# Kernel optimization log

Hardware: AMD Instinct MI355X
Metric: run time of the kernel (lower is better)

The kernel has to match this reference:

```python
import jax, jax.numpy as jnp
import numpy as np

DN = ('NCHW', 'OIHW', 'NCHW')

def _convlstm_scan(x, W, b):
    """x: [S,B,Cin,H,W]; W: [4*Co, Cin+Co, 3, 3]; b: [4*Co]. Returns all h: [S,B,Co,H,W]."""
    S, B, Cin, H, Wd = x.shape
    Co = W.shape[0] // 4
    h0 = jnp.zeros((B, Co, H, Wd), x.dtype)
    c0 = jnp.zeros((B, Co, H, Wd), x.dtype)

    def step(carry, xt):
        h, c = carry
        z = jax.lax.conv_general_dilated(
            jnp.concatenate([xt, h], axis=1), W,
            window_strides=(1, 1), padding='SAME', dimension_numbers=DN)
        z = z + b[None, :, None, None]
        i, f, o, g = jnp.split(z, 4, axis=1)
        c = jax.nn.sigmoid(f) * c + jax.nn.sigmoid(i) * jnp.tanh(g)
        h = jax.nn.sigmoid(o) * jnp.tanh(c)
        return (h, c), h

    _, outs = jax.lax.scan(step, (h0, c0), x)
    return outs


def setup_inputs() -> dict:
    key = jax.random.key(0)
    k1, k2, k3 = jax.random.split(key, 3)
    S, B, C, H, W = 16, 4, 32, 128, 128
    Co = 32
    x = jax.random.normal(k1, (S, B, C, H, W), dtype=jnp.float32)
    Wf = jax.random.normal(k2, (4 * Co, C + Co, 3, 3), dtype=jnp.float32) * 0.05
    bf = jnp.zeros((4 * Co,), dtype=jnp.float32)
    Wb = jax.random.normal(k3, (4 * Co, C + Co, 3, 3), dtype=jnp.float32) * 0.05
    bb = jnp.zeros((4 * Co,), dtype=jnp.float32)
    return {"x": x, "Wf": Wf, "bf": bf, "Wb": Wb, "bb": bb}


def reference(x, Wf, bf, Wb, bb):
    fwd_outs = _convlstm_scan(x, Wf, bf)            # [S,B,Co,H,W]
    bwd_outs = _convlstm_scan(x[::-1], Wb, bb)      # [S,B,Co,H,W] (time-reversed input)
    # Faithful to source: backward outputs concatenated WITHOUT re-flipping.
    return jnp.concatenate([fwd_outs, bwd_outs], axis=2)  # [S,B,2*Co,H,W]
```

## Files before the change

### kernel.cpp

```cpp
#include <hip/hip_runtime.h>

#define S_ 16
#define B_ 4
#define H_ 128
#define W_ 128
#define HW_ (H_ * W_)
#define NPOS 324
#define TILE_ELEMS (NPOS * 32)

typedef __attribute__((ext_vector_type(8))) _Float16 half8;
typedef __attribute__((ext_vector_type(4))) _Float16 half4;
typedef __attribute__((ext_vector_type(4))) float f32x4;

__device__ __forceinline__ float sigf(float x) { return 1.f / (1.f + __expf(-x)); }
__device__ __forceinline__ float tanhf_(float x) { return 2.f / (1.f + __expf(-2.f * x)) - 1.f; }

__device__ __forceinline__ void gl2lds16(const _Float16* g, _Float16* l) {
    __builtin_amdgcn_global_load_lds(
        (const __attribute__((address_space(1))) unsigned int*)g,
        (__attribute__((address_space(3))) unsigned int*)l, 16, 0, 0);
}

__global__ void prep_pack(const float* __restrict__ Wf, const float* __restrict__ Wb,
                          _Float16* __restrict__ wpk) {
    int id = blockIdx.x * 256 + threadIdx.x;
    if (id >= 18432) return;
    int l = id & 63;
    int nf = (id >> 6) & 7;
    int ks = (id >> 9) % 18;
    int d = id / 9216;
    const float* Wsrc = d ? Wb : Wf;
    int tap = ks >> 1, half = ks & 1;
    int dy = tap / 3, dx = tap - dy * 3;
    int co = nf * 16 + (l & 15);
    _Float16* dst = wpk + (size_t)d * 73728 + ((size_t)(ks * 8 + nf) * 64 + l) * 8;
#pragma unroll
    for (int e = 0; e < 8; ++e) {
        int ci = half * 32 + (l >> 4) * 8 + e;
        dst[e] = (_Float16)Wsrc[((co * 64 + ci) * 3 + dy) * 3 + dx];
    }
}

__global__ void prep_xtiles(const float* __restrict__ x, _Float16* __restrict__ xt) {
    int id = blockIdx.x * 256 + threadIdx.x;
    if (id >= 16 * 4 * 64 * NPOS * 4) return;
    int cb = id & 3;
    int u = id >> 2;
    int pos = u % NPOS;
    int v = u / NPOS;
    int tile = v & 63;
    v >>= 6;
    int b = v & 3;
    int ts = v >> 2;
    int r = pos / 18, cc = pos - r * 18;
    int gy = (tile >> 3) * 16 + r - 1;
    int gx = (tile & 7) * 16 + cc - 1;
    bool inb = ((unsigned)gy < 128u) && ((unsigned)gx < 128u);
    const float* g = x + ((size_t)(ts * 4 + b) * 32 + cb * 8) * HW_ + (size_t)gy * W_ + gx;
    half8 vv;
#pragma unroll
    for (int e = 0; e < 8; ++e)
        vv[e] = inb ? (_Float16)__builtin_nontemporal_load(g + e * HW_) : (_Float16)0.f;
    *(half8*)(xt + (size_t)u * 32 + cb * 8) = vv;
}

__device__ __forceinline__ half8 lda(const _Float16* __restrict__ base, int m, int dy,
                                     int dx, int px, int kg, int wq) {
    return *(const half8*)(base + (size_t)(((wq * 4 + m + dy) * 18) + px + dx) * 32 + kg * 8);
}
__device__ __forceinline__ half8 ldb(const _Float16* __restrict__ bw, int ks, int nf, int lane) {
    return *(const half8*)(bw + (size_t)(ks * 8 + nf) * 512 + lane * 8);
}

__global__ __launch_bounds__(256, 2)
void convlstm_step(const _Float16* __restrict__ xtiles,
                   const _Float16* __restrict__ hin,
                   _Float16* __restrict__ hout,
                   const _Float16* __restrict__ wpk,
                   const float* __restrict__ biasf, const float* __restrict__ biasb,
                   _Float16* __restrict__ cst,
                   float* __restrict__ out, int t) {
    const int tile = blockIdx.x;
    const int dirb = blockIdx.y;
    const int dir = dirb >> 2, b = dirb & 3;
    const int ts = dir ? (S_ - 1 - t) : t;

    const _Float16* base_x = xtiles + ((size_t)(ts * 4 + b) * 64 + tile) * TILE_ELEMS;
    const _Float16* base_h = hin + ((size_t)dirb * 64 + tile) * TILE_ELEMS;
    _Float16* hob = hout + (size_t)dirb * 64 * TILE_ELEMS;
    const _Float16* bw = wpk + (size_t)dir * 73728;
    const float* bias = dir ? biasb : biasf;
    _Float16* cbase = cst + (size_t)dirb * 32 * HW_;
    float* outp = out + ((size_t)(t * 4 + b) * 64 + dir * 32) * HW_;

    __shared__ alignas(16) _Float16 bsh[2][2][8][64][8];

    const int tid = threadIdx.x;
    const int lane = tid & 63, wq = tid >> 6;
    const int px = lane & 15, kg = lane >> 4;

    f32x4 acc[4][8];
#pragma unroll
    for (int m = 0; m < 4; ++m)
#pragma unroll
        for (int nf = 0; nf < 8; ++nf) acc[m][nf] = (f32x4)(0.f);

    if (t == 0) {
#pragma unroll 1
        for (int tap = 0; tap < 9; ++tap) {
            int dy = tap / 3, dx = tap - dy * 3;
            half8 a[4];
#pragma unroll
            for (int m = 0; m < 4; ++m) a[m] = lda(base_x, m, dy, dx, px, kg, wq);
#pragma unroll
            for (int nf = 0; nf < 8; ++nf) {
                half8 bb8 = ldb(bw, tap * 2, nf, lane);
#pragma unroll
                for (int m = 0; m < 4; ++m)
                    acc[m][nf] = __builtin_amdgcn_mfma_f32_16x16x32_f16(a[m], bb8, acc[m][nf], 0, 0, 0);
            }
        }
    } else {
        half8 aP[2][4], aQ[2][4];
        {
#pragma unroll
            for (int j = 0; j < 4; ++j) {
                int f = wq * 4 + j;
                int hf = f >> 3, nf = f & 7;
                gl2lds16(bw + (size_t)(hf * 8 + nf) * 512 + lane * 8, &bsh[0][hf][nf][0][0]);
            }
#pragma unroll
            for (int m = 0; m < 4; ++m) {
                aP[0][m] = lda(base_x, m, 0, 0, px, kg, wq);
                aP[1][m] = lda(base_h, m, 0, 0, px, kg, wq);
            }
        }

        auto body = [&](int tap, half8(&acur)[2][4], half8(&anxt)[2][4]) {
            __syncthreads();
            if (tap < 8) {
                const int tn = tap + 1;
                const int dyn_ = tn / 3, dxn = tn - dyn_ * 3;
#pragma unroll
                for (int j = 0; j < 4; ++j) {
                    int f = wq * 4 + j;
                    int hf = f >> 3, nf = f & 7;
                    gl2lds16(bw + (size_t)((tn * 2 + hf) * 8 + nf) * 512 + lane * 8,
                             &bsh[tn & 1][hf][nf][0][0]);
                }
#pragma unroll
                for (int m = 0; m < 4; ++m) {
                    anxt[0][m] = lda(base_x, m, dyn_, dxn, px, kg, wq);
                    anxt[1][m] = lda(base_h, m, dyn_, dxn, px, kg, wq);
                }
            }
            const _Float16* lb = &bsh[tap & 1][0][0][0][0];
#pragma unroll
            for (int hf = 0; hf < 2; ++hf) {
#pragma unroll
                for (int nf = 0; nf < 8; ++nf) {
                    half8 bb8 = *(const half8*)(lb + (size_t)(hf * 8 + nf) * 512 + lane * 8);
#pragma unroll
                    for (int m = 0; m < 4; ++m)
                        acc[m][nf] = __builtin_amdgcn_mfma_f32_16x16x32_f16(acur[hf][m], bb8, acc[m][nf], 0, 0, 0);
                }
            }
        };
#pragma unroll 1
        for (int tap = 0; tap < 9; tap += 2) {
            body(tap, aP, aQ);
            if (tap + 1 < 9) body(tap + 1, aQ, aP);
        }
    }

    const int q0 = px;
    const int gx0 = (tile & 7) * 16, gy0 = (tile >> 3) * 16;
    const int tx = tile & 7, ty_ = tile >> 3;
    const int lx0 = kg * 4;

    float bI[2], bF[2], bO[2], bG[2];
#pragma unroll
    for (int qs = 0; qs < 2; ++qs) {
        bI[qs] = bias[qs * 16 + q0];
        bF[qs] = bias[32 + qs * 16 + q0];
        bO[qs] = bias[64 + qs * 16 + q0];
        bG[qs] = bias[96 + qs * 16 + q0];
    }
#pragma unroll
    for (int m = 0; m < 4; ++m) {
        const int ly = wq * 4 + m;
        const int gy = gy0 + ly;
#pragma unroll
        for (int qs = 0; qs < 2; ++qs) {
            const int q = qs * 16 + q0;
            f32x4 zi = acc[m][qs], zf = acc[m][2 + qs], zo = acc[m][4 + qs], zg = acc[m][6 + qs];
            size_t off = (size_t)q * HW_ + (size_t)gy * W_ + gx0 + lx0;
            half4 cold4 = (half4)((_Float16)0.f);
            if (t) cold4 = *(const half4*)(cbase + off);
            half4 cn4;
            f32x4 hn;
#pragma unroll
            for (int r = 0; r < 4; ++r) {
                float I = sigf(zi[r] + bI[qs]);
                float F = sigf(zf[r] + bF[qs]);
                float O = sigf(zo[r] + bO[qs]);
                float G = tanhf_(zg[r] + bG[qs]);
                float cnr = F * (float)cold4[r] + I * G;
                cn4[r] = (_Float16)cnr;
                hn[r] = O * tanhf_(cnr);
            }
            *(half4*)(cbase + off) = cn4;
            __builtin_nontemporal_store(hn, (f32x4*)(outp + off));
#pragma unroll
            for (int r = 0; r < 4; ++r) {
                _Float16 hh = (_Float16)hn[r];
                int lx = lx0 + r;
                hob[((size_t)tile) * TILE_ELEMS + (size_t)((ly + 1) * 18 + lx + 1) * 32 + q] = hh;
                bool Le = (lx == 0) && (tx > 0);
                bool Re = (lx == 15) && (tx < 7);
                bool Te = (ly == 0) && (ty_ > 0);
                bool Be = (ly == 15) && (ty_ < 7);
                if (Le) hob[((size_t)tile - 1) * TILE_ELEMS + (size_t)((ly + 1) * 18 + 17) * 32 + q] = hh;
                if (Re) hob[((size_t)tile + 1) * TILE_ELEMS + (size_t)((ly + 1) * 18 + 0) * 32 + q] = hh;
                if (Te) hob[((size_t)tile - 8) * TILE_ELEMS + (size_t)(17 * 18 + lx + 1) * 32 + q] = hh;
                if (Be) hob[((size_t)tile + 8) * TILE_ELEMS + (size_t)(0 * 18 + lx + 1) * 32 + q] = hh;
                if (Te && Le) hob[((size_t)tile - 9) * TILE_ELEMS + (size_t)(17 * 18 + 17) * 32 + q] = hh;
                if (Te && Re) hob[((size_t)tile - 7) * TILE_ELEMS + (size_t)(17 * 18 + 0) * 32 + q] = hh;
                if (Be && Le) hob[((size_t)tile + 7) * TILE_ELEMS + (size_t)(0 * 18 + 17) * 32 + q] = hh;
                if (Be && Re) hob[((size_t)tile + 9) * TILE_ELEMS + (size_t)(0 * 18 + 0) * 32 + q] = hh;
            }
        }
    }
}

extern "C" void kernel_launch(void* const* d_in, const int* in_sizes, int n_in,
                              void* d_out, int out_size, void* d_ws, size_t ws_size,
                              hipStream_t stream) {
    const float* x  = (const float*)d_in[0];
    const float* Wf = (const float*)d_in[1];
    const float* bf = (const float*)d_in[2];
    const float* Wb = (const float*)d_in[3];
    const float* bb = (const float*)d_in[4];
    float* out = (float*)d_out;
    char* ws = (char*)d_ws;

    const size_t OFF_WPK = 0;
    const size_t OFF_XT  = 327680;
    const size_t OFF_H0  = OFF_XT + 84934656;
    const size_t OFF_H1  = OFF_H0 + 10616832;
    const size_t OFF_C   = OFF_H1 + 10616832;

    _Float16* wpk = (_Float16*)(ws + OFF_WPK);
    _Float16* xt  = (_Float16*)(ws + OFF_XT);
    _Float16* hb[2] = { (_Float16*)(ws + OFF_H0), (_Float16*)(ws + OFF_H1) };
    _Float16* cst = (_Float16*)(ws + OFF_C);

    hipMemsetAsync(ws + OFF_H0, 0, 2u * 10616832u, stream);

    prep_pack<<<dim3(72), dim3(256), 0, stream>>>(Wf, Wb, wpk);
    prep_xtiles<<<dim3(20736), dim3(256), 0, stream>>>(x, xt);

    for (int t = 0; t < S_; ++t) {
        convlstm_step<<<dim3(64, 8), dim3(256), 0, stream>>>(
            xt, hb[(t + 1) & 1], hb[t & 1], wpk, bf, bb, cst, out, t);
    }
}
```

Before: 683.6 us.

## Widen tiles to 16x32 with 512 threads and preload full weights into LDS

Spatial tiles grow from 16x16 to 16x32 pixels, so the halo overhead in the padded x and h tiles shrinks and there are half as many blocks, each with 8 waves. All 18 weight k-slices (144KB) are copied into dynamic LDS once at kernel start, which removes the per-tap barriers and the double-buffered weight streaming. The A operands are prefetched four slices ahead in registers. In exchange only one block fits per CU, and the grid is 256 blocks, so occupancy and latency hiding go down while register pressure goes up.

```diff
diff --git a/kernel.cpp b/kernel.cpp
--- a/kernel.cpp
+++ b/kernel.cpp
@@ -5,7 +5,9 @@
 #define H_ 128
 #define W_ 128
 #define HW_ (H_ * W_)
-#define NPOS 324
+#define AH 18
+#define AW 34
+#define NPOS (AH * AW)
 #define TILE_ELEMS (NPOS * 32)
 
 typedef __attribute__((ext_vector_type(8))) _Float16 half8;
@@ -43,18 +45,18 @@
 
 __global__ void prep_xtiles(const float* __restrict__ x, _Float16* __restrict__ xt) {
     int id = blockIdx.x * 256 + threadIdx.x;
-    if (id >= 16 * 4 * 64 * NPOS * 4) return;
+    if (id >= 16 * 4 * 32 * NPOS * 4) return;
     int cb = id & 3;
     int u = id >> 2;
     int pos = u % NPOS;
     int v = u / NPOS;
-    int tile = v & 63;
-    v >>= 6;
+    int tile = v & 31;
+    v >>= 5;
     int b = v & 3;
     int ts = v >> 2;
-    int r = pos / 18, cc = pos - r * 18;
-    int gy = (tile >> 3) * 16 + r - 1;
-    int gx = (tile & 7) * 16 + cc - 1;
+    int ar = pos / AW, ac = pos - ar * AW;
+    int gy = (tile >> 2) * 16 + ar - 1;
+    int gx = (tile & 3) * 32 + ac - 1;
     bool inb = ((unsigned)gy < 128u) && ((unsigned)gx < 128u);
     const float* g = x + ((size_t)(ts * 4 + b) * 32 + cb * 8) * HW_ + (size_t)gy * W_ + gx;
     half8 vv;
@@ -64,15 +66,15 @@
     *(half8*)(xt + (size_t)u * 32 + cb * 8) = vv;
 }
 
-__device__ __forceinline__ half8 lda(const _Float16* __restrict__ base, int m, int dy,
+__device__ __forceinline__ half8 lda(const _Float16* __restrict__ base, int f, int dy,
                                      int dx, int px, int kg, int wq) {
-    return *(const half8*)(base + (size_t)(((wq * 4 + m + dy) * 18) + px + dx) * 32 + kg * 8);
-}
-__device__ __forceinline__ half8 ldb(const _Float16* __restrict__ bw, int ks, int nf, int lane) {
-    return *(const half8*)(bw + (size_t)(ks * 8 + nf) * 512 + lane * 8);
-}
-
-__global__ __launch_bounds__(256, 2)
+    int pos = (wq * 2 + (f >> 1) + dy) * AW + (f & 1) * 16 + px + dx;
+    return *(const half8*)(base + (size_t)pos * 32 + kg * 8);
+}
+
+extern __shared__ _Float16 bsh[];
+
+__global__ __launch_bounds__(512, 1)
 void convlstm_step(const _Float16* __restrict__ xtiles,
                    const _Float16* __restrict__ hin,
                    _Float16* __restrict__ hout,
@@ -85,97 +87,91 @@
     const int dir = dirb >> 2, b = dirb & 3;
     const int ts = dir ? (S_ - 1 - t) : t;
 
-    const _Float16* base_x = xtiles + ((size_t)(ts * 4 + b) * 64 + tile) * TILE_ELEMS;
-    const _Float16* base_h = hin + ((size_t)dirb * 64 + tile) * TILE_ELEMS;
-    _Float16* hob = hout + (size_t)dirb * 64 * TILE_ELEMS;
+    const _Float16* base_x = xtiles + ((size_t)(ts * 4 + b) * 32 + tile) * TILE_ELEMS;
+    const _Float16* base_h = hin + ((size_t)dirb * 32 + tile) * TILE_ELEMS;
+    _Float16* hob = hout + (size_t)dirb * 32 * TILE_ELEMS;
     const _Float16* bw = wpk + (size_t)dir * 73728;
     const float* bias = dir ? biasb : biasf;
     _Float16* cbase = cst + (size_t)dirb * 32 * HW_;
     float* outp = out + ((size_t)(t * 4 + b) * 64 + dir * 32) * HW_;
 
-    __shared__ alignas(16) _Float16 bsh[2][2][8][64][8];
-
     const int tid = threadIdx.x;
     const int lane = tid & 63, wq = tid >> 6;
     const int px = lane & 15, kg = lane >> 4;
 
+#pragma unroll
+    for (int k = 0; k < 18; ++k) {
+        int wb = k * 512 + (tid & ~63);
+        gl2lds16(bw + ((size_t)wb + lane) * 8, bsh + (size_t)wb * 8);
+    }
+
     f32x4 acc[4][8];
 #pragma unroll
-    for (int m = 0; m < 4; ++m)
-#pragma unroll
-        for (int nf = 0; nf < 8; ++nf) acc[m][nf] = (f32x4)(0.f);
+    for (int f = 0; f < 4; ++f)
+#pragma unroll
+        for (int nf = 0; nf < 8; ++nf) acc[f][nf] = (f32x4)(0.f);
+
+    half8 abuf[4][4];
 
     if (t == 0) {
-#pragma unroll 1
+#pragma unroll
+        for (int tp = 0; tp < 4; ++tp) {
+            int dy = tp / 3, dx = tp - dy * 3;
+#pragma unroll
+            for (int f = 0; f < 4; ++f) abuf[tp][f] = lda(base_x, f, dy, dx, px, kg, wq);
+        }
+        __syncthreads();
+#pragma unroll
         for (int tap = 0; tap < 9; ++tap) {
-            int dy = tap / 3, dx = tap - dy * 3;
-            half8 a[4];
-#pragma unroll
-            for (int m = 0; m < 4; ++m) a[m] = lda(base_x, m, dy, dx, px, kg, wq);
+            const int slot = tap & 3;
 #pragma unroll
             for (int nf = 0; nf < 8; ++nf) {
-                half8 bb8 = ldb(bw, tap * 2, nf, lane);
-#pragma unroll
-                for (int m = 0; m < 4; ++m)
-                    acc[m][nf] = __builtin_amdgcn_mfma_f32_16x16x32_f16(a[m], bb8, acc[m][nf], 0, 0, 0);
+                half8 b8 = *(const half8*)(bsh + ((size_t)((tap * 2) * 8 + nf) << 9) + (lane << 3));
+#pragma unroll
+                for (int f = 0; f < 4; ++f)
+                    acc[f][nf] = __builtin_amdgcn_mfma_f32_16x16x32_f16(abuf[slot][f], b8, acc[f][nf], 0, 0, 0);
+            }
+            if (tap + 4 < 9) {
+                const int tn = tap + 4;
+                const int dyn_ = tn / 3, dxn = tn - dyn_ * 3;
+#pragma unroll
+                for (int f = 0; f < 4; ++f) abuf[slot][f] = lda(base_x, f, dyn_, dxn, px, kg, wq);
             }
         }
     } else {
-        half8 aP[2][4], aQ[2][4];
-        {
-#pragma unroll
-            for (int j = 0; j < 4; ++j) {
-                int f = wq * 4 + j;
-                int hf = f >> 3, nf = f & 7;
-                gl2lds16(bw + (size_t)(hf * 8 + nf) * 512 + lane * 8, &bsh[0][hf][nf][0][0]);
-            }
-#pragma unroll
-            for (int m = 0; m < 4; ++m) {
-                aP[0][m] = lda(base_x, m, 0, 0, px, kg, wq);
-                aP[1][m] = lda(base_h, m, 0, 0, px, kg, wq);
-            }
-        }
-
-        auto body = [&](int tap, half8(&acur)[2][4], half8(&anxt)[2][4]) {
-            __syncthreads();
-            if (tap < 8) {
-                const int tn = tap + 1;
+#pragma unroll
+        for (int k0 = 0; k0 < 4; ++k0) {
+            int tp = k0 >> 1;
+            int dy = tp / 3, dx = tp - dy * 3;
+            const _Float16* src = (k0 & 1) ? base_h : base_x;
+#pragma unroll
+            for (int f = 0; f < 4; ++f) abuf[k0][f] = lda(src, f, dy, dx, px, kg, wq);
+        }
+        __syncthreads();
+#pragma unroll
+        for (int ks = 0; ks < 18; ++ks) {
+            const int slot = ks & 3;
+#pragma unroll
+            for (int nf = 0; nf < 8; ++nf) {
+                half8 b8 = *(const half8*)(bsh + ((size_t)(ks * 8 + nf) << 9) + (lane << 3));
+#pragma unroll
+                for (int f = 0; f < 4; ++f)
+                    acc[f][nf] = __builtin_amdgcn_mfma_f32_16x16x32_f16(abuf[slot][f], b8, acc[f][nf], 0, 0, 0);
+            }
+            if (ks + 4 < 18) {
+                const int kn = ks + 4;
+                const int tn = kn >> 1;
                 const int dyn_ = tn / 3, dxn = tn - dyn_ * 3;
-#pragma unroll
-                for (int j = 0; j < 4; ++j) {
-                    int f = wq * 4 + j;
-                    int hf = f >> 3, nf = f & 7;
-                    gl2lds16(bw + (size_t)((tn * 2 + hf) * 8 + nf) * 512 + lane * 8,
-                             &bsh[tn & 1][hf][nf][0][0]);
-                }
-#pragma unroll
-                for (int m = 0; m < 4; ++m) {
-                    anxt[0][m] = lda(base_x, m, dyn_, dxn, px, kg, wq);
-                    anxt[1][m] = lda(base_h, m, dyn_, dxn, px, kg, wq);
-                }
-            }
-            const _Float16* lb = &bsh[tap & 1][0][0][0][0];
-#pragma unroll
-            for (int hf = 0; hf < 2; ++hf) {
-#pragma unroll
-                for (int nf = 0; nf < 8; ++nf) {
-                    half8 bb8 = *(const half8*)(lb + (size_t)(hf * 8 + nf) * 512 + lane * 8);
-#pragma unroll
-                    for (int m = 0; m < 4; ++m)
-                        acc[m][nf] = __builtin_amdgcn_mfma_f32_16x16x32_f16(acur[hf][m], bb8, acc[m][nf], 0, 0, 0);
-                }
-            }
-        };
-#pragma unroll 1
-        for (int tap = 0; tap < 9; tap += 2) {
-            body(tap, aP, aQ);
-            if (tap + 1 < 9) body(tap + 1, aQ, aP);
+                const _Float16* src = (kn & 1) ? base_h : base_x;
+#pragma unroll
+                for (int f = 0; f < 4; ++f) abuf[slot][f] = lda(src, f, dyn_, dxn, px, kg, wq);
+            }
         }
     }
 
     const int q0 = px;
-    const int gx0 = (tile & 7) * 16, gy0 = (tile >> 3) * 16;
-    const int tx = tile & 7, ty_ = tile >> 3;
+    const int gx0 = (tile & 3) * 32, gy0 = (tile >> 2) * 16;
+    const int tx = tile & 3, ty_ = tile >> 2;
     const int lx0 = kg * 4;
 
     float bI[2], bF[2], bO[2], bG[2];
@@ -187,14 +183,15 @@
         bG[qs] = bias[96 + qs * 16 + q0];
     }
 #pragma unroll
-    for (int m = 0; m < 4; ++m) {
-        const int ly = wq * 4 + m;
-        const int gy = gy0 + ly;
+    for (int f = 0; f < 4; ++f) {
+        const int row = wq * 2 + (f >> 1);
+        const int gy = gy0 + row;
+        const int colb = (f & 1) * 16 + lx0;
 #pragma unroll
         for (int qs = 0; qs < 2; ++qs) {
             const int q = qs * 16 + q0;
-            f32x4 zi = acc[m][qs], zf = acc[m][2 + qs], zo = acc[m][4 + qs], zg = acc[m][6 + qs];
-            size_t off = (size_t)q * HW_ + (size_t)gy * W_ + gx0 + lx0;
+            f32x4 zi = acc[f][qs], zf = acc[f][2 + qs], zo = acc[f][4 + qs], zg = acc[f][6 + qs];
+            size_t off = (size_t)q * HW_ + (size_t)gy * W_ + gx0 + colb;
             half4 cold4 = (half4)((_Float16)0.f);
             if (t) cold4 = *(const half4*)(cbase + off);
             half4 cn4;
@@ -214,20 +211,20 @@
 #pragma unroll
             for (int r = 0; r < 4; ++r) {
                 _Float16 hh = (_Float16)hn[r];
-                int lx = lx0 + r;
-                hob[((size_t)tile) * TILE_ELEMS + (size_t)((ly + 1) * 18 + lx + 1) * 32 + q] = hh;
-                bool Le = (lx == 0) && (tx > 0);
-                bool Re = (lx == 15) && (tx < 7);
-                bool Te = (ly == 0) && (ty_ > 0);
-                bool Be = (ly == 15) && (ty_ < 7);
-                if (Le) hob[((size_t)tile - 1) * TILE_ELEMS + (size_t)((ly + 1) * 18 + 17) * 32 + q] = hh;
-                if (Re) hob[((size_t)tile + 1) * TILE_ELEMS + (size_t)((ly + 1) * 18 + 0) * 32 + q] = hh;
-                if (Te) hob[((size_t)tile - 8) * TILE_ELEMS + (size_t)(17 * 18 + lx + 1) * 32 + q] = hh;
-                if (Be) hob[((size_t)tile + 8) * TILE_ELEMS + (size_t)(0 * 18 + lx + 1) * 32 + q] = hh;
-                if (Te && Le) hob[((size_t)tile - 9) * TILE_ELEMS + (size_t)(17 * 18 + 17) * 32 + q] = hh;
-                if (Te && Re) hob[((size_t)tile - 7) * TILE_ELEMS + (size_t)(17 * 18 + 0) * 32 + q] = hh;
-                if (Be && Le) hob[((size_t)tile + 7) * TILE_ELEMS + (size_t)(0 * 18 + 17) * 32 + q] = hh;
-                if (Be && Re) hob[((size_t)tile + 9) * TILE_ELEMS + (size_t)(0 * 18 + 0) * 32 + q] = hh;
+                int col = colb + r;
+                hob[(size_t)tile * TILE_ELEMS + (size_t)((row + 1) * AW + col + 1) * 32 + q] = hh;
+                bool Le = (col == 0) && (tx > 0);
+                bool Re = (col == 31) && (tx < 3);
+                bool Te = (row == 0) && (ty_ > 0);
+                bool Be = (row == 15) && (ty_ < 7);
+                if (Le) hob[(size_t)(tile - 1) * TILE_ELEMS + (size_t)((row + 1) * AW + 33) * 32 + q] = hh;
+                if (Re) hob[(size_t)(tile + 1) * TILE_ELEMS + (size_t)((row + 1) * AW + 0) * 32 + q] = hh;
+                if (Te) hob[(size_t)(tile - 4) * TILE_ELEMS + (size_t)(17 * AW + col + 1) * 32 + q] = hh;
+                if (Be) hob[(size_t)(tile + 4) * TILE_ELEMS + (size_t)(0 * AW + col + 1) * 32 + q] = hh;
+                if (Te && Le) hob[(size_t)(tile - 5) * TILE_ELEMS + (size_t)(17 * AW + 33) * 32 + q] = hh;
+                if (Te && Re) hob[(size_t)(tile - 3) * TILE_ELEMS + (size_t)(17 * AW + 0) * 32 + q] = hh;
+                if (Be && Le) hob[(size_t)(tile + 3) * TILE_ELEMS + (size_t)(0 * AW + 33) * 32 + q] = hh;
+                if (Be && Re) hob[(size_t)(tile + 5) * TILE_ELEMS + (size_t)(0 * AW + 0) * 32 + q] = hh;
             }
         }
     }
@@ -246,22 +243,25 @@
 
     const size_t OFF_WPK = 0;
     const size_t OFF_XT  = 327680;
-    const size_t OFF_H0  = OFF_XT + 84934656;
-    const size_t OFF_H1  = OFF_H0 + 10616832;
-    const size_t OFF_C   = OFF_H1 + 10616832;
+    const size_t OFF_H0  = OFF_XT + 80216064;
+    const size_t OFF_H1  = OFF_H0 + 10027008;
+    const size_t OFF_C   = OFF_H1 + 10027008;
 
     _Float16* wpk = (_Float16*)(ws + OFF_WPK);
     _Float16* xt  = (_Float16*)(ws + OFF_XT);
     _Float16* hb[2] = { (_Float16*)(ws + OFF_H0), (_Float16*)(ws + OFF_H1) };
     _Float16* cst = (_Float16*)(ws + OFF_C);
 
-    hipMemsetAsync(ws + OFF_H0, 0, 2u * 10616832u, stream);
+    hipFuncSetAttribute((const void*)convlstm_step,
+                        hipFuncAttributeMaxDynamicSharedMemorySize, 147456);
+
+    hipMemsetAsync(ws + OFF_H0, 0, 2u * 10027008u, stream);
 
     prep_pack<<<dim3(72), dim3(256), 0, stream>>>(Wf, Wb, wpk);
-    prep_xtiles<<<dim3(20736), dim3(256), 0, stream>>>(x, xt);
+    prep_xtiles<<<dim3(19584), dim3(256), 0, stream>>>(x, xt);
 
     for (int t = 0; t < S_; ++t) {
-        convlstm_step<<<dim3(64, 8), dim3(256), 0, stream>>>(
+        convlstm_step<<<dim3(32, 8), dim3(512), 147456, stream>>>(
             xt, hb[(t + 1) & 1], hb[t & 1], wpk, bf, bb, cst, out, t);
     }
 }
```

Result: faster. 608.1 us (-11.0%).
